# Kernel tuning notes

Hardware: AMD Instinct MI355X
Metric: run time of the kernel (lower is better)

Reference implementation:

```python
import jax, jax.numpy as jnp
import numpy as np

B, S, H = 2, 2048, 2304
NH, NKV, HD = 8, 4, 256
FF = 9216
SOFTCAP = 50.0
SCALE = 256.0 ** -0.5  # query_pre_attn_scalar ** -0.5
EPS = 1e-6
THETA = 10000.0


def setup_inputs() -> dict:
    key = jax.random.key(0)
    ks = jax.random.split(key, 13)
    s = 0.02
    x = jax.random.normal(ks[0], (B, S, H), jnp.float32)
    causal = jnp.tril(jnp.ones((S, S), bool))
    mask = jnp.where(causal, 0.0, -1e9).astype(jnp.float32)[None, None]  # [1,1,S,S]
    return {
        "x": x,
        "mask": mask,
        "wq": jax.random.normal(ks[1], (H, NH * HD), jnp.float32) * s,
        "wk": jax.random.normal(ks[2], (H, NKV * HD), jnp.float32) * s,
        "wv": jax.random.normal(ks[3], (H, NKV * HD), jnp.float32) * s,
        "wo": jax.random.normal(ks[4], (NH * HD, H), jnp.float32) * s,
        "w_gate": jax.random.normal(ks[5], (H, FF), jnp.float32) * s,
        "w_up": jax.random.normal(ks[6], (H, FF), jnp.float32) * s,
        "w_down": jax.random.normal(ks[7], (FF, H), jnp.float32) * s,
        "g_in": jax.random.normal(ks[8], (H,), jnp.float32) * 0.1,
        "g_post_attn": jax.random.normal(ks[9], (H,), jnp.float32) * 0.1,
        "g_pre_ff": jax.random.normal(ks[10], (H,), jnp.float32) * 0.1,
        "g_post_ff": jax.random.normal(ks[11], (H,), jnp.float32) * 0.1,
    }


def rmsnorm(x, g):
    # Gemma2RMSNorm: fp32 norm, (1 + weight) gain
    x32 = x.astype(jnp.float32)
    var = jnp.mean(x32 * x32, axis=-1, keepdims=True)
    return (x32 * jax.lax.rsqrt(var + EPS) * (1.0 + g.astype(jnp.float32))).astype(x.dtype)


def apply_rope(q, k):
    # q: [B,S,NH,HD], k: [B,S,NKV,HD]; positions 0..S-1 (start_pos=0)
    inv_freq = 1.0 / (THETA ** (jnp.arange(0, HD, 2, dtype=jnp.float32) / HD))
    t = jnp.arange(S, dtype=jnp.float32)
    freqs = jnp.outer(t, inv_freq)                 # [S, HD/2]
    emb = jnp.concatenate([freqs, freqs], axis=-1)  # [S, HD]
    cos = jnp.cos(emb)[None, :, None, :]
    sin = jnp.sin(emb)[None, :, None, :]

    def rot_half(v):
        return jnp.concatenate([-v[..., HD // 2:], v[..., : HD // 2]], axis=-1)

    return q * cos + rot_half(q) * sin, k * cos + rot_half(k) * sin


def reference(x, mask, wq, wk, wv, wo, w_gate, w_up, w_down,
              g_in, g_post_attn, g_pre_ff, g_post_ff):
    # --- attention sub-block ---
    h = rmsnorm(x, g_in)
    q = (h @ wq).reshape(B, S, NH, HD)
    k = (h @ wk).reshape(B, S, NKV, HD)
    v = (h @ wv).reshape(B, S, NKV, HD)
    q, k = apply_rope(q, k)
    rep = NH // NKV
    k = jnp.repeat(k, rep, axis=2)  # [B,S,NH,HD]
    v = jnp.repeat(v, rep, axis=2)
    scores = jnp.einsum('bqhd,bkhd->bhqk', q, k) * SCALE
    scores = SOFTCAP * jnp.tanh(scores / SOFTCAP)  # logit soft-capping
    scores = scores + mask
    p = jax.nn.softmax(scores, axis=-1)
    o = jnp.einsum('bhqk,bkhd->bqhd', p, v).reshape(B, S, NH * HD)
    attn_out = o @ wo
    h2 = x + rmsnorm(attn_out, g_post_attn)
    # --- GeGLU MLP sub-block ---
    f = rmsnorm(h2, g_pre_ff)
    mlp = (jax.nn.gelu(f @ w_gate, approximate=True) * (f @ w_up)) @ w_down
    return h2 + rmsnorm(mlp, g_post_ff)
```

## Files before the change

kernel.cpp:

```cpp
#include <hip/hip_runtime.h>
#include <hip/hip_bf16.h>
#include <cstdint>
#include <cstddef>

typedef __bf16 bf16;
typedef __bf16 bf16x8 __attribute__((ext_vector_type(8)));
typedef __bf16 bf16x4v __attribute__((ext_vector_type(4)));
typedef float f32x4 __attribute__((ext_vector_type(4)));

#define NB 2
#define NS 2048
#define NHID 2304
#define NHEADS 8
#define NKVH 4
#define HDIM 256
#define NFF 9216
#define NROWS (NB * NS)
#define SCALE_F 0.0625f
#define SOFTCAP_F 50.0f

#define ASYNC16(ldsp, gp)                                                     \
    __builtin_amdgcn_global_load_lds(                                         \
        (__attribute__((address_space(1))) void*)(gp),                        \
        (__attribute__((address_space(3))) void*)(ldsp), 16, 0, 0)

__device__ __forceinline__ float fast_tanh(float x) {
    x = fminf(fmaxf(x, -10.f), 10.f);
    float e = __expf(2.f * x);
    return (e - 1.f) / (e + 1.f);
}

__global__ __launch_bounds__(256)
void transpose_cvt_part(const float* __restrict__ W, int N, int k0,
                        bf16* __restrict__ dst, int dstK, int dstOff) {
    __shared__ float tile[64][65];
    const int ntiles = N >> 6;
    const int tk = blockIdx.x / ntiles, tn = blockIdx.x % ntiles;
    const int kk0 = k0 + (tk << 6), n0 = tn << 6;
    const int tr = threadIdx.x >> 4, tc = threadIdx.x & 15;
#pragma unroll
    for (int j = 0; j < 4; ++j) {
        const int r = j * 16 + tr;
        const float4 v = *(const float4*)&W[(size_t)(kk0 + r) * N + n0 + tc * 4];
        tile[r][tc * 4 + 0] = v.x; tile[r][tc * 4 + 1] = v.y;
        tile[r][tc * 4 + 2] = v.z; tile[r][tc * 4 + 3] = v.w;
    }
    __syncthreads();
#pragma unroll
    for (int j = 0; j < 4; ++j) {
        const int n = j * 16 + tr;
        bf16x4v o;
        o.x = (bf16)tile[tc * 4 + 0][n];
        o.y = (bf16)tile[tc * 4 + 1][n];
        o.z = (bf16)tile[tc * 4 + 2][n];
        o.w = (bf16)tile[tc * 4 + 3][n];
        *(bf16x4v*)&dst[(size_t)(n0 + n) * dstK + dstOff + (tk << 6) + tc * 4] = o;
    }
}

__global__ __launch_bounds__(256)
void copy_expand(const bf16* __restrict__ src, bf16* __restrict__ dst,
                 int srcK, int dstK, int total) {
    const int idx = blockIdx.x * 256 + threadIdx.x;
    if (idx >= total) return;
    const int cpr = srcK >> 3;
    const int n = idx / cpr, c = idx % cpr;
    *(uint4*)&dst[(size_t)n * dstK + c * 8] = *(const uint4*)&src[(size_t)n * srcK + c * 8];
}

template <bool ADD, bool OBF>
__global__ __launch_bounds__(256)
void rmsnorm_k(const float* __restrict__ src, const float* __restrict__ res,
               const float* __restrict__ g, void* __restrict__ out) {
    const int row = blockIdx.x;
    const float* xr = src + (size_t)row * NHID;
    float vals[9];
    float ss = 0.f;
#pragma unroll
    for (int j = 0; j < 9; ++j) {
        vals[j] = xr[threadIdx.x + j * 256];
        ss += vals[j] * vals[j];
    }
#pragma unroll
    for (int off = 32; off > 0; off >>= 1) ss += __shfl_xor(ss, off);
    __shared__ float wss[4];
    if ((threadIdx.x & 63) == 0) wss[threadIdx.x >> 6] = ss;
    __syncthreads();
    const float scale = rsqrtf((wss[0] + wss[1] + wss[2] + wss[3]) * (1.f / NHID) + 1e-6f);
#pragma unroll
    for (int j = 0; j < 9; ++j) {
        const int c = threadIdx.x + j * 256;
        float v = vals[j] * scale * (1.f + g[c]);
        if constexpr (ADD) v += res[(size_t)row * NHID + c];
        if constexpr (OBF) ((bf16*)out)[(size_t)row * NHID + c] = (bf16)v;
        else               ((float*)out)[(size_t)row * NHID + c] = v;
    }
}

__global__ __launch_bounds__(256)
void rope_k(bf16* __restrict__ q, bf16* __restrict__ k) {
    const int idx = blockIdx.x * 256 + threadIdx.x;
    const int i = idx & 127;
    const int t = idx >> 7;
    const int head = t % 12;
    const int row = t / 12;
    const int s = row & (NS - 1);
    const float ang = (float)s * exp2f(-(float)i * 0.10381025296523007f);
    float sn, cs;
    sincosf(ang, &sn, &cs);
    bf16* base = (head < 8) ? (q + (size_t)row * 2048 + head * 256 + i)
                            : (k + (size_t)row * 1024 + (head - 8) * 256 + i);
    const float x1 = (float)base[0], x2 = (float)base[128];
    base[0]   = (bf16)(x1 * cs - x2 * sn);
    base[128] = (bf16)(x2 * cs + x1 * sn);
}

template <int MODE>
__global__ __launch_bounds__(256)
void gemm_bt(const bf16* __restrict__ A, const bf16* __restrict__ Bt,
             void* __restrict__ C, int M, int N, int K) {
    __shared__ __align__(16) bf16 As[128 * 32];
    __shared__ __align__(16) bf16 Bs[128 * 32];
    const int tid = threadIdx.x;
    const int lane = tid & 63, wave = tid >> 6;
    const int lq = lane & 15, quad = lane >> 4;
    const int ntiles = N >> 7;
    const int tm = blockIdx.x / ntiles, tn = blockIdx.x % ntiles;
    const int m0 = tm << 7, n0 = tn << 7;
    const int wrow = (wave >> 1) << 6, wcol = (wave & 1) << 6;
    f32x4 acc[4][4];
#pragma unroll
    for (int i = 0; i < 4; ++i)
#pragma unroll
        for (int j = 0; j < 4; ++j) acc[i][j] = (f32x4){0.f, 0.f, 0.f, 0.f};

    const int wr0 = wave * 32;
    const int lrow = lane >> 2, lcol = (lane & 3) * 8;

    for (int k0 = 0; k0 < K; k0 += 32) {
        __syncthreads();
        const bf16* ga = &A[(size_t)(m0 + wr0 + lrow) * K + k0 + lcol];
        const bf16* gb = &Bt[(size_t)(n0 + wr0 + lrow) * K + k0 + lcol];
#pragma unroll
        for (int j = 0; j < 2; ++j) {
            ASYNC16(&As[(wr0 + j * 16) * 32], ga + (size_t)(j * 16) * K);
            ASYNC16(&Bs[(wr0 + j * 16) * 32], gb + (size_t)(j * 16) * K);
        }
        __syncthreads();
        bf16x8 af[4], bfr[4];
#pragma unroll
        for (int i = 0; i < 4; ++i) {
            af[i]  = *(const bf16x8*)&As[(wrow + i * 16 + lq) * 32 + quad * 8];
            bfr[i] = *(const bf16x8*)&Bs[(wcol + i * 16 + lq) * 32 + quad * 8];
        }
#pragma unroll
        for (int mi = 0; mi < 4; ++mi)
#pragma unroll
            for (int ni = 0; ni < 4; ++ni)
                acc[mi][ni] = __builtin_amdgcn_mfma_f32_16x16x32_bf16(af[mi], bfr[ni], acc[mi][ni], 0, 0, 0);
    }
#pragma unroll
    for (int mi = 0; mi < 4; ++mi) {
        const int r0 = m0 + wrow + mi * 16 + quad * 4;
#pragma unroll
        for (int ni = 0; ni < 4; ++ni) {
            const int cc = n0 + wcol + ni * 16 + lq;
#pragma unroll
            for (int i = 0; i < 4; ++i) {
                const float v = acc[mi][ni][i];
                if constexpr (MODE == 0) {
                    ((float*)C)[(size_t)(r0 + i) * N + cc] = v;
                } else if constexpr (MODE == 1) {
                    ((bf16*)C)[(size_t)(r0 + i) * N + cc] = (bf16)v;
                } else {
                    const int m = r0 + i, bb = m >> 11, ss = m & 2047;
                    ((bf16*)C)[((size_t)bb * N + cc) * 2048 + ss] = (bf16)v;
                }
            }
        }
    }
}

__global__ __launch_bounds__(256, 2)
void geglu_gemm(const bf16* __restrict__ A, const bf16* __restrict__ Bg,
                const bf16* __restrict__ Bu, bf16* __restrict__ C,
                int M, int N, int K) {
    __shared__ __align__(16) bf16 As[128 * 32];
    __shared__ __align__(16) bf16 Bs[128 * 32];
    const int tid = threadIdx.x;
    const int lane = tid & 63, wave = tid >> 6;
    const int lq = lane & 15, quad = lane >> 4;
    const int ntiles = N >> 7;
    const int tm = blockIdx.x / ntiles, tn = blockIdx.x % ntiles;
    const int m0 = tm << 7, n0 = tn << 7;
    const int wrow = (wave >> 1) << 6, wcol = (wave & 1) << 6;
    const int wr0 = wave * 32;
    const int lrow = lane >> 2, lcol = (lane & 3) * 8;

    f32x4 acc[4][4];
    bf16x4v gelv[4][4];

#pragma unroll
    for (int i = 0; i < 4; ++i)
#pragma unroll
        for (int j = 0; j < 4; ++j) acc[i][j] = (f32x4){0.f, 0.f, 0.f, 0.f};

    for (int k0 = 0; k0 < K; k0 += 32) {
        __syncthreads();
        const bf16* ga = &A[(size_t)(m0 + wr0 + lrow) * K + k0 + lcol];
        const bf16* gb = &Bg[(size_t)(n0 + wr0 + lrow) * K + k0 + lcol];
#pragma unroll
        for (int j = 0; j < 2; ++j) {
            ASYNC16(&As[(wr0 + j * 16) * 32], ga + (size_t)(j * 16) * K);
            ASYNC16(&Bs[(wr0 + j * 16) * 32], gb + (size_t)(j * 16) * K);
        }
        __syncthreads();
        bf16x8 af[4], bfr[4];
#pragma unroll
        for (int i = 0; i < 4; ++i) {
            af[i]  = *(const bf16x8*)&As[(wrow + i * 16 + lq) * 32 + quad * 8];
            bfr[i] = *(const bf16x8*)&Bs[(wcol + i * 16 + lq) * 32 + quad * 8];
        }
#pragma unroll
        for (int mi = 0; mi < 4; ++mi)
#pragma unroll
            for (int ni = 0; ni < 4; ++ni)
                acc[mi][ni] = __builtin_amdgcn_mfma_f32_16x16x32_bf16(af[mi], bfr[ni], acc[mi][ni], 0, 0, 0);
    }

#pragma unroll
    for (int mi = 0; mi < 4; ++mi)
#pragma unroll
        for (int ni = 0; ni < 4; ++ni) {
#pragma unroll
            for (int i = 0; i < 4; ++i) {
                const float gx = acc[mi][ni][i];
                const float inner = 0.7978845608028654f * (gx + 0.044715f * gx * gx * gx);
                gelv[mi][ni][i] = (bf16)(0.5f * gx * (1.f + fast_tanh(inner)));
            }
            acc[mi][ni] = (f32x4){0.f, 0.f, 0.f, 0.f};
        }

    for (int k0 = 0; k0 < K; k0 += 32) {
        __syncthreads();
        const bf16* ga = &A[(size_t)(m0 + wr0 + lrow) * K + k0 + lcol];
        const bf16* gb = &Bu[(size_t)(n0 + wr0 + lrow) * K + k0 + lcol];
#pragma unroll
        for (int j = 0; j < 2; ++j) {
            ASYNC16(&As[(wr0 + j * 16) * 32], ga + (size_t)(j * 16) * K);
            ASYNC16(&Bs[(wr0 + j * 16) * 32], gb + (size_t)(j * 16) * K);
        }
        __syncthreads();
        bf16x8 af[4], bfr[4];
#pragma unroll
        for (int i = 0; i < 4; ++i) {
            af[i]  = *(const bf16x8*)&As[(wrow + i * 16 + lq) * 32 + quad * 8];
            bfr[i] = *(const bf16x8*)&Bs[(wcol + i * 16 + lq) * 32 + quad * 8];
        }
#pragma unroll
        for (int mi = 0; mi < 4; ++mi)
#pragma unroll
            for (int ni = 0; ni < 4; ++ni)
                acc[mi][ni] = __builtin_amdgcn_mfma_f32_16x16x32_bf16(af[mi], bfr[ni], acc[mi][ni], 0, 0, 0);
    }

#pragma unroll
    for (int mi = 0; mi < 4; ++mi) {
        const int r0 = m0 + wrow + mi * 16 + quad * 4;
#pragma unroll
        for (int ni = 0; ni < 4; ++ni) {
            const int cc = n0 + wcol + ni * 16 + lq;
#pragma unroll
            for (int i = 0; i < 4; ++i)
                C[(size_t)(r0 + i) * N + cc] = (bf16)((float)gelv[mi][ni][i] * acc[mi][ni][i]);
        }
    }
}

__global__ __launch_bounds__(256)
void attn_k(const bf16* __restrict__ Q, const bf16* __restrict__ Kb,
            const bf16* __restrict__ Vt, bf16* __restrict__ O) {
    const int qt = blockIdx.x & 31;
    const int bh = blockIdx.x >> 5;
    const int h = bh & 7, b = bh >> 3;
    const int kvh = h >> 1;
    const int tid = threadIdx.x, lane = tid & 63, wave = tid >> 6;
    const int lq = lane & 15, quad = lane >> 4;

    __shared__ __align__(16) bf16 Ks[32 * 264];
    __shared__ __align__(16) bf16 VTs[256 * 40];
    __shared__ __align__(16) bf16 Ps[64 * 40];

    const bf16* qbase = Q + ((size_t)(b * NS + qt * 64)) * 2048 + h * 256;
    const bf16* kbase = Kb + (size_t)(b * NS) * 1024 + kvh * 256;
    const bf16* vbase = Vt + (size_t)b * 1024 * 2048 + (size_t)(kvh * 256) * 2048;

    bf16x8 aq[8];
#pragma unroll
    for (int ks = 0; ks < 8; ++ks)
        aq[ks] = *(const bf16x8*)&qbase[(size_t)(wave * 16 + lq) * 2048 + ks * 32 + quad * 8];

    f32x4 acco[16];
#pragma unroll
    for (int i = 0; i < 16; ++i) acco[i] = (f32x4){0.f, 0.f, 0.f, 0.f};
    float m_old[4] = {-1e30f, -1e30f, -1e30f, -1e30f};
    float l_old[4] = {0.f, 0.f, 0.f, 0.f};

    const int ktmax = 2 * qt + 1;
    for (int kt = 0; kt <= ktmax; ++kt) {
        __syncthreads();
#pragma unroll
        for (int j = 0; j < 4; ++j) {
            const int c = j * 256 + tid;
            const int r = c >> 5, c8 = (c & 31) * 8;
            *(uint4*)&Ks[r * 264 + c8] = *(const uint4*)&kbase[(size_t)(kt * 32 + r) * 1024 + c8];
        }
#pragma unroll
        for (int j = 0; j < 4; ++j) {
            const int c = j * 256 + tid;
            const int d = c >> 2, s8 = (c & 3) * 8;
            *(uint4*)&VTs[d * 40 + s8] = *(const uint4*)&vbase[(size_t)d * 2048 + kt * 32 + s8];
        }
        __syncthreads();

        f32x4 accs[2];
        accs[0] = (f32x4){0.f, 0.f, 0.f, 0.f};
        accs[1] = (f32x4){0.f, 0.f, 0.f, 0.f};
#pragma unroll
        for (int ks = 0; ks < 8; ++ks) {
#pragma unroll
            for (int nt = 0; nt < 2; ++nt) {
                const bf16x8 bk = *(const bf16x8*)&Ks[(nt * 16 + lq) * 264 + ks * 32 + quad * 8];
                accs[nt] = __builtin_amdgcn_mfma_f32_16x16x32_bf16(aq[ks], bk, accs[nt], 0, 0, 0);
            }
        }

        const bool diag = (kt >= 2 * qt);
        float p[2][4], rmax[4], rsum[4];
#pragma unroll
        for (int i = 0; i < 4; ++i) rmax[i] = -1e30f;
#pragma unroll
        for (int nt = 0; nt < 2; ++nt)
#pragma unroll
            for (int i = 0; i < 4; ++i) {
                float v = accs[nt][i] * SCALE_F;
                v = SOFTCAP_F * fast_tanh(v * (1.f / SOFTCAP_F));
                if (diag) {
                    const int qabs = qt * 64 + wave * 16 + quad * 4 + i;
                    const int kabs = kt * 32 + nt * 16 + lq;
                    if (kabs > qabs) v = -1e30f;
                }
                p[nt][i] = v;
                rmax[i] = fmaxf(rmax[i], v);
            }
#pragma unroll
        for (int i = 0; i < 4; ++i)
#pragma unroll
            for (int off = 8; off; off >>= 1) rmax[i] = fmaxf(rmax[i], __shfl_xor(rmax[i], off));

        float alpha[4];
#pragma unroll
        for (int i = 0; i < 4; ++i) {
            const float mn = fmaxf(m_old[i], rmax[i]);
            alpha[i] = __expf(m_old[i] - mn);
            m_old[i] = mn;
            rsum[i] = 0.f;
        }
#pragma unroll
        for (int nt = 0; nt < 2; ++nt)
#pragma unroll
            for (int i = 0; i < 4; ++i) {
                const float e = __expf(p[nt][i] - m_old[i]);
                p[nt][i] = e;
                rsum[i] += e;
            }
#pragma unroll
        for (int i = 0; i < 4; ++i) {
#pragma unroll
            for (int off = 8; off; off >>= 1) rsum[i] += __shfl_xor(rsum[i], off);
            l_old[i] = l_old[i] * alpha[i] + rsum[i];
        }
#pragma unroll
        for (int dt = 0; dt < 16; ++dt)
#pragma unroll
            for (int i = 0; i < 4; ++i) acco[dt][i] *= alpha[i];

#pragma unroll
        for (int nt = 0; nt < 2; ++nt)
#pragma unroll
            for (int i = 0; i < 4; ++i)
                Ps[(wave * 16 + quad * 4 + i) * 40 + nt * 16 + lq] = (bf16)p[nt][i];

        const bf16x8 ap = *(const bf16x8*)&Ps[(wave * 16 + lq) * 40 + quad * 8];
#pragma unroll
        for (int dt = 0; dt < 16; ++dt) {
            const bf16x8 bv = *(const bf16x8*)&VTs[(dt * 16 + lq) * 40 + quad * 8];
            acco[dt] = __builtin_amdgcn_mfma_f32_16x16x32_bf16(ap, bv, acco[dt], 0, 0, 0);
        }
    }

    bf16* obase = O + ((size_t)(b * NS + qt * 64 + wave * 16)) * 2048 + h * 256;
    float linv[4];
#pragma unroll
    for (int i = 0; i < 4; ++i) linv[i] = 1.f / l_old[i];
#pragma unroll
    for (int dt = 0; dt < 16; ++dt)
#pragma unroll
        for (int i = 0; i < 4; ++i)
            obase[(size_t)(quad * 4 + i) * 2048 + dt * 16 + lq] = (bf16)(acco[dt][i] * linv[i]);
}

extern "C" void kernel_launch(void* const* d_in, const int* in_sizes, int n_in,
                              void* d_out, int out_size, void* d_ws, size_t ws_size,
                              hipStream_t stream) {
    const float* x    = (const float*)d_in[0];
    float* wq   = (float*)d_in[2];
    float* wk   = (float*)d_in[3];
    float* wv   = (float*)d_in[4];
    float* wo   = (float*)d_in[5];
    float* wg   = (float*)d_in[6];
    float* wu   = (float*)d_in[7];
    float* wd   = (float*)d_in[8];
    const float* g_in = (const float*)d_in[9];
    const float* g_pa = (const float*)d_in[10];
    const float* g_pf = (const float*)d_in[11];
    const float* g_po = (const float*)d_in[12];
    float* out = (float*)d_out;

    uint8_t* ws = (uint8_t*)d_ws;
    size_t off = 0;
    auto alloc = [&](size_t bytes) {
        void* p = ws + off;
        off += (bytes + 255) & ~(size_t)255;
        return p;
    };
    bf16* temp   = (bf16*)alloc((size_t)9216 * 1152 * 2);
    bf16* h_bf   = (bf16*)alloc((size_t)NROWS * 2304 * 2);
    uint8_t* R   = (uint8_t*)alloc((size_t)NROWS * 9216 * 2);
    float* tmp1  = (float*)alloc((size_t)NROWS * 2304 * 4);
    float* h2    = (float*)alloc((size_t)NROWS * 2304 * 4);
    (void)ws_size; (void)in_sizes; (void)n_in; (void)out_size;

    bf16* q_bf   = (bf16*)R;
    bf16* k_bf   = (bf16*)(R + (size_t)16777216);
    bf16* v_t    = (bf16*)(R + (size_t)16777216 + 8388608);
    bf16* o_bf   = (bf16*)(R + (size_t)16777216 + 2 * 8388608);
    bf16* mlp_in = (bf16*)R;

    auto convert_weight = [&](float* W, int K, int N) {
        const int hK = K >> 1;
        const int blks = (hK >> 6) * (N >> 6);
        transpose_cvt_part<<<blks, 256, 0, stream>>>(W, N, 0, temp, hK, 0);
        transpose_cvt_part<<<blks, 256, 0, stream>>>(W, N, hK, (bf16*)W, K, hK);
        const int total = N * (hK >> 3);
        copy_expand<<<(total + 255) / 256, 256, 0, stream>>>(temp, (bf16*)W, hK, K, total);
    };
    convert_weight(wq, 2304, 2048);
    convert_weight(wk, 2304, 1024);
    convert_weight(wv, 2304, 1024);
    convert_weight(wo, 2048, 2304);
    convert_weight(wg, 2304, 9216);
    convert_weight(wu, 2304, 9216);
    convert_weight(wd, 9216, 2304);
    const bf16* wq_t = (const bf16*)wq;
    const bf16* wk_t = (const bf16*)wk;
    const bf16* wv_t = (const bf16*)wv;
    const bf16* wo_t = (const bf16*)wo;
    const bf16* wg_t = (const bf16*)wg;
    const bf16* wu_t = (const bf16*)wu;
    const bf16* wd_t = (const bf16*)wd;

    rmsnorm_k<false, true><<<NROWS, 256, 0, stream>>>(x, nullptr, g_in, h_bf);

    gemm_bt<1><<<32 * 16, 256, 0, stream>>>(h_bf, wq_t, q_bf, NROWS, 2048, 2304);
    gemm_bt<1><<<32 * 8, 256, 0, stream>>>(h_bf, wk_t, k_bf, NROWS, 1024, 2304);
    gemm_bt<2><<<32 * 8, 256, 0, stream>>>(h_bf, wv_t, v_t, NROWS, 1024, 2304);

    rope_k<<<(NROWS * 12 * 128) / 256, 256, 0, stream>>>(q_bf, k_bf);

    attn_k<<<NB * NHEADS * (NS / 64), 256, 0, stream>>>(q_bf, k_bf, v_t, o_bf);

    gemm_bt<0><<<32 * 18, 256, 0, stream>>>(o_bf, wo_t, tmp1, NROWS, 2304, 2048);

    rmsnorm_k<true, false><<<NROWS, 256, 0, stream>>>(tmp1, x, g_pa, h2);
    rmsnorm_k<false, true><<<NROWS, 256, 0, stream>>>(h2, nullptr, g_pf, h_bf);

    geglu_gemm<<<32 * 72, 256, 0, stream>>>(h_bf, wg_t, wu_t, mlp_in, NROWS, 9216, 2304);

    gemm_bt<0><<<32 * 18, 256, 0, stream>>>(mlp_in, wd_t, tmp1, NROWS, 2304, 9216);

    rmsnorm_k<true, false><<<NROWS, 256, 0, stream>>>(tmp1, h2, g_po, (void*)out);
}
```

Before: 1.687 ms.

## Add triple-buffered 256x128 swizzled GEMM with XCD remap; split GeGLU into two passes

Adds a new GEMM kernel with 512 threads and 256x128 tiles. It triple-buffers 64-wide K slices in LDS using async global-to-LDS loads, an XOR-swizzled LDS layout and partial vmcnt waits, and remaps blocks across the XCDs. The Q projection and the GeGLU MLP now use it. The fused gate/up kernel is replaced by two launches: one writes gelu(gate) to mlp_in, and the second multiplies the up projection by that stored gate in place. This adds an extra bf16 round-trip of the 4096x9216 intermediate in exchange for better load overlap and data reuse.

Result: no change. 1.690 ms (+0.1%).

```diff
diff --git a/kernel.cpp b/kernel.cpp
--- a/kernel.cpp
+++ b/kernel.cpp
@@ -181,98 +181,118 @@
     }
 }
 
-__global__ __launch_bounds__(256, 2)
-void geglu_gemm(const bf16* __restrict__ A, const bf16* __restrict__ Bg,
-                const bf16* __restrict__ Bu, bf16* __restrict__ C,
-                int M, int N, int K) {
-    __shared__ __align__(16) bf16 As[128 * 32];
-    __shared__ __align__(16) bf16 Bs[128 * 32];
+__device__ __forceinline__ int ldsoff(int row, int s) {
+    return (row << 6) + (((s ^ row) & 7) << 3);
+}
+
+__device__ __forceinline__ void stage_tile(const bf16* __restrict__ Ag,
+                                           const bf16* __restrict__ Bg,
+                                           bf16* as, bf16* bs,
+                                           int K, int k0, int w, int l) {
+    const int rsub = l >> 3;
+    const int koff = k0 + (((l & 7) ^ rsub) << 3);
+    const int r0 = w * 8 + rsub;
+#pragma unroll
+    for (int c = 0; c < 4; ++c)
+        ASYNC16(as + (c * 64 + w * 8) * 64, &Ag[(size_t)(c * 64 + r0) * K + koff]);
+#pragma unroll
+    for (int c = 0; c < 2; ++c)
+        ASYNC16(bs + (c * 64 + w * 8) * 64, &Bg[(size_t)(c * 64 + r0) * K + koff]);
+}
+
+template <int MODE>
+__global__ __launch_bounds__(512, 2)
+void gemm256(const bf16* __restrict__ A, const bf16* __restrict__ Bt,
+             void* __restrict__ C, const bf16* __restrict__ gate,
+             int M, int N, int K) {
+    __shared__ __align__(16) bf16 lds[3 * 24576];
     const int tid = threadIdx.x;
-    const int lane = tid & 63, wave = tid >> 6;
-    const int lq = lane & 15, quad = lane >> 4;
-    const int ntiles = N >> 7;
-    const int tm = blockIdx.x / ntiles, tn = blockIdx.x % ntiles;
-    const int m0 = tm << 7, n0 = tn << 7;
-    const int wrow = (wave >> 1) << 6, wcol = (wave & 1) << 6;
-    const int wr0 = wave * 32;
-    const int lrow = lane >> 2, lcol = (lane & 3) * 8;
+    const int l = tid & 63, w = tid >> 6;
+    const int lq = l & 15, quad = l >> 4;
+    const int wm = w >> 1, wn = w & 1;
+
+    const int ntm = M >> 8;
+    const int nwg = gridDim.x, bid = blockIdx.x;
+    const int q8 = nwg >> 3, r8 = nwg & 7;
+    const int xcd = bid & 7, loc = bid >> 3;
+    const int wg = (xcd < r8 ? xcd * (q8 + 1) : r8 * (q8 + 1) + (xcd - r8) * q8) + loc;
+    const int tm = wg % ntm, tn = wg / ntm;
+
+    const bf16* Ab = A  + (size_t)(tm << 8) * K;
+    const bf16* Bb = Bt + (size_t)(tn << 7) * K;
+
+    const int NT = K >> 6;
+    stage_tile(Ab, Bb, lds, lds + 16384, K, 0, w, l);
+    stage_tile(Ab, Bb, lds + 24576, lds + 24576 + 16384, K, 64, w, l);
+    asm volatile("s_waitcnt vmcnt(6)" ::: "memory");
+    __builtin_amdgcn_s_barrier();
+    __builtin_amdgcn_sched_barrier(0);
 
     f32x4 acc[4][4];
-    bf16x4v gelv[4][4];
-
 #pragma unroll
     for (int i = 0; i < 4; ++i)
 #pragma unroll
         for (int j = 0; j < 4; ++j) acc[i][j] = (f32x4){0.f, 0.f, 0.f, 0.f};
 
-    for (int k0 = 0; k0 < K; k0 += 32) {
-        __syncthreads();
-        const bf16* ga = &A[(size_t)(m0 + wr0 + lrow) * K + k0 + lcol];
-        const bf16* gb = &Bg[(size_t)(n0 + wr0 + lrow) * K + k0 + lcol];
-#pragma unroll
-        for (int j = 0; j < 2; ++j) {
-            ASYNC16(&As[(wr0 + j * 16) * 32], ga + (size_t)(j * 16) * K);
-            ASYNC16(&Bs[(wr0 + j * 16) * 32], gb + (size_t)(j * 16) * K);
-        }
-        __syncthreads();
-        bf16x8 af[4], bfr[4];
-#pragma unroll
-        for (int i = 0; i < 4; ++i) {
-            af[i]  = *(const bf16x8*)&As[(wrow + i * 16 + lq) * 32 + quad * 8];
-            bfr[i] = *(const bf16x8*)&Bs[(wcol + i * 16 + lq) * 32 + quad * 8];
-        }
-#pragma unroll
-        for (int mi = 0; mi < 4; ++mi)
-#pragma unroll
-            for (int ni = 0; ni < 4; ++ni)
-                acc[mi][ni] = __builtin_amdgcn_mfma_f32_16x16x32_bf16(af[mi], bfr[ni], acc[mi][ni], 0, 0, 0);
-    }
-
-#pragma unroll
-    for (int mi = 0; mi < 4; ++mi)
+    int b = 0;
+    for (int t = 0; t < NT; ++t) {
+        bf16* as = lds + b * 24576;
+        bf16* bs = as + 16384;
+        if (t + 2 < NT) {
+            int b2 = b + 2; if (b2 >= 3) b2 -= 3;
+            stage_tile(Ab, Bb, lds + b2 * 24576, lds + b2 * 24576 + 16384,
+                       K, (t + 2) << 6, w, l);
+        }
+#pragma unroll
+        for (int kk = 0; kk < 2; ++kk) {
+            bf16x8 af[4], bfr[4];
+#pragma unroll
+            for (int i = 0; i < 4; ++i)
+                af[i]  = *(const bf16x8*)&as[ldsoff(wm * 64 + i * 16 + lq, kk * 4 + quad)];
+#pragma unroll
+            for (int i = 0; i < 4; ++i)
+                bfr[i] = *(const bf16x8*)&bs[ldsoff(wn * 64 + i * 16 + lq, kk * 4 + quad)];
+            __builtin_amdgcn_s_setprio(1);
+#pragma unroll
+            for (int mi = 0; mi < 4; ++mi)
+#pragma unroll
+                for (int ni = 0; ni < 4; ++ni)
+                    acc[mi][ni] = __builtin_amdgcn_mfma_f32_16x16x32_bf16(
+                        af[mi], bfr[ni], acc[mi][ni], 0, 0, 0);
+            __builtin_amdgcn_s_setprio(0);
+        }
+        if (t + 1 < NT) {
+            if (t + 2 < NT) { asm volatile("s_waitcnt vmcnt(6)" ::: "memory"); }
+            else            { asm volatile("s_waitcnt vmcnt(0)" ::: "memory"); }
+            __builtin_amdgcn_s_barrier();
+            __builtin_amdgcn_sched_barrier(0);
+        }
+        if (++b == 3) b = 0;
+    }
+
+    const int r0base = (tm << 8) + wm * 64 + quad * 4;
+    const int c0base = (tn << 7) + wn * 64 + lq;
+#pragma unroll
+    for (int mi = 0; mi < 4; ++mi) {
 #pragma unroll
         for (int ni = 0; ni < 4; ++ni) {
+            const int cc = c0base + ni * 16;
 #pragma unroll
             for (int i = 0; i < 4; ++i) {
-                const float gx = acc[mi][ni][i];
-                const float inner = 0.7978845608028654f * (gx + 0.044715f * gx * gx * gx);
-                gelv[mi][ni][i] = (bf16)(0.5f * gx * (1.f + fast_tanh(inner)));
+                const int rr = r0base + mi * 16 + i;
+                const size_t idx = (size_t)rr * N + cc;
+                const float v = acc[mi][ni][i];
+                if constexpr (MODE == 0) {
+                    ((float*)C)[idx] = v;
+                } else if constexpr (MODE == 1) {
+                    ((bf16*)C)[idx] = (bf16)v;
+                } else if constexpr (MODE == 3) {
+                    const float inner = 0.7978845608028654f * (v + 0.044715f * v * v * v);
+                    ((bf16*)C)[idx] = (bf16)(0.5f * v * (1.f + fast_tanh(inner)));
+                } else {
+                    ((bf16*)C)[idx] = (bf16)((float)gate[idx] * v);
+                }
             }
-            acc[mi][ni] = (f32x4){0.f, 0.f, 0.f, 0.f};
-        }
-
-    for (int k0 = 0; k0 < K; k0 += 32) {
-        __syncthreads();
-        const bf16* ga = &A[(size_t)(m0 + wr0 + lrow) * K + k0 + lcol];
-        const bf16* gb = &Bu[(size_t)(n0 + wr0 + lrow) * K + k0 + lcol];
-#pragma unroll
-        for (int j = 0; j < 2; ++j) {
-            ASYNC16(&As[(wr0 + j * 16) * 32], ga + (size_t)(j * 16) * K);
-            ASYNC16(&Bs[(wr0 + j * 16) * 32], gb + (size_t)(j * 16) * K);
-        }
-        __syncthreads();
-        bf16x8 af[4], bfr[4];
-#pragma unroll
-        for (int i = 0; i < 4; ++i) {
-            af[i]  = *(const bf16x8*)&As[(wrow + i * 16 + lq) * 32 + quad * 8];
-            bfr[i] = *(const bf16x8*)&Bs[(wcol + i * 16 + lq) * 32 + quad * 8];
-        }
-#pragma unroll
-        for (int mi = 0; mi < 4; ++mi)
-#pragma unroll
-            for (int ni = 0; ni < 4; ++ni)
-                acc[mi][ni] = __builtin_amdgcn_mfma_f32_16x16x32_bf16(af[mi], bfr[ni], acc[mi][ni], 0, 0, 0);
-    }
-
-#pragma unroll
-    for (int mi = 0; mi < 4; ++mi) {
-        const int r0 = m0 + wrow + mi * 16 + quad * 4;
-#pragma unroll
-        for (int ni = 0; ni < 4; ++ni) {
-            const int cc = n0 + wcol + ni * 16 + lq;
-#pragma unroll
-            for (int i = 0; i < 4; ++i)
-                C[(size_t)(r0 + i) * N + cc] = (bf16)((float)gelv[mi][ni][i] * acc[mi][ni][i]);
         }
     }
 }
@@ -472,7 +492,7 @@
 
     rmsnorm_k<false, true><<<NROWS, 256, 0, stream>>>(x, nullptr, g_in, h_bf);
 
-    gemm_bt<1><<<32 * 16, 256, 0, stream>>>(h_bf, wq_t, q_bf, NROWS, 2048, 2304);
+    gemm256<1><<<16 * 16, 512, 0, stream>>>(h_bf, wq_t, q_bf, nullptr, NROWS, 2048, 2304);
     gemm_bt<1><<<32 * 8, 256, 0, stream>>>(h_bf, wk_t, k_bf, NROWS, 1024, 2304);
     gemm_bt<2><<<32 * 8, 256, 0, stream>>>(h_bf, wv_t, v_t, NROWS, 1024, 2304);
 
@@ -485,7 +505,8 @@
     rmsnorm_k<true, false><<<NROWS, 256, 0, stream>>>(tmp1, x, g_pa, h2);
     rmsnorm_k<false, true><<<NROWS, 256, 0, stream>>>(h2, nullptr, g_pf, h_bf);
 
-    geglu_gemm<<<32 * 72, 256, 0, stream>>>(h_bf, wg_t, wu_t, mlp_in, NROWS, 9216, 2304);
+    gemm256<3><<<16 * 72, 512, 0, stream>>>(h_bf, wg_t, mlp_in, nullptr, NROWS, 9216, 2304);
+    gemm256<4><<<16 * 72, 512, 0, stream>>>(h_bf, wu_t, mlp_in, mlp_in, NROWS, 9216, 2304);
 
     gemm_bt<0><<<32 * 18, 256, 0, stream>>>(mlp_in, wd_t, tmp1, NROWS, 2304, 9216);
 
```
